# Kernel tuning notes

Hardware: AMD Instinct MI355X
Metric: run time of the kernel (lower is better)

The kernel has to match this reference:

```python
import jax, jax.numpy as jnp
import numpy as np

N = 8192
F_IN = 512
F_HID = 256
ALPHA = 0.2  # LeakyReLU negative slope
NEG_INF = -9e15


def gat_layer(h, adj, W, a):
    """Standard dense GraphAttentionLayer (pyGAT style).
    h: [N, F_in], adj: [N, N] (0/1), W: [F_in, F_out], a: [2*F_out, 1].
    """
    Wh = h @ W  # [N, F_out]
    f_out = W.shape[1]
    # e_ij = leakyrelu(a1 . Wh_i + a2 . Wh_j) via broadcasting
    e1 = Wh @ a[:f_out]      # [N, 1]
    e2 = Wh @ a[f_out:]      # [N, 1]
    e = jax.nn.leaky_relu(e1 + e2.T, negative_slope=ALPHA)  # [N, N]
    e = jnp.where(adj > 0, e, NEG_INF)
    att = jax.nn.softmax(e, axis=-1)  # masked row softmax
    return jax.nn.elu(att @ Wh)       # [N, F_out]


def setup_inputs() -> dict:
    key = jax.random.key(0)
    k_x, k_adj, k_w1, k_a1, k_w2, k_a2 = jax.random.split(key, 6)
    x = jax.random.normal(k_x, (N, F_IN), dtype=jnp.float32)
    # sparse random adjacency (~avg degree 16) + self loops
    adj = (jax.random.uniform(k_adj, (N, N)) < (16.0 / N)).astype(jnp.float32)
    adj = jnp.clip(adj + jnp.eye(N, dtype=jnp.float32), 0.0, 1.0)
    # Xavier-ish init for layer params
    W1 = jax.random.normal(k_w1, (F_IN, F_HID), dtype=jnp.float32) * (1.0 / np.sqrt(F_IN))
    a1 = jax.random.normal(k_a1, (2 * F_HID, 1), dtype=jnp.float32) * (1.0 / np.sqrt(2 * F_HID))
    W2 = jax.random.normal(k_w2, (F_HID, F_IN), dtype=jnp.float32) * (1.0 / np.sqrt(F_HID))
    a2 = jax.random.normal(k_a2, (2 * F_IN, 1), dtype=jnp.float32) * (1.0 / np.sqrt(2 * F_IN))
    return {"x": x, "adj": adj, "W1": W1, "a1": a1, "W2": W2, "a2": a2}


def reference(x, adj, W1, a1, W2, a2):
    enc = gat_layer(x, adj, W1, a1)    # encode: [N, F_HID]
    dec = gat_layer(enc, adj, W2, a2)  # decode: [N, F_IN]
    return (dec, enc)
```

## Files before the change

kernel.cpp:

```cpp
#include <hip/hip_runtime.h>
#include <hip/hip_bf16.h>

#define N_NODES 8192
#define F_IN    512
#define F_HID   256
#define ALPHA   0.2f
#define MAXDEG  64

using f32x4 = __attribute__((ext_vector_type(4))) float;
using f16x8 = __attribute__((ext_vector_type(8))) _Float16;
using f16x4 = __attribute__((ext_vector_type(4))) _Float16;

__global__ void conv_WT(const float* __restrict__ W1, const float* __restrict__ W2,
                        _Float16* __restrict__ W1T, _Float16* __restrict__ W2T,
                        const float* __restrict__ a2,
                        float* __restrict__ w2s, float* __restrict__ w2t,
                        float* __restrict__ stz) {
    const int tid = threadIdx.x;
    int gid = blockIdx.x * 256 + tid;
    if (gid < 2 * N_NODES) stz[gid] = 0.0f;

    if (blockIdx.x >= 256) {
        const int r = (blockIdx.x - 256) * 64 + (tid >> 2);
        const int q = tid & 3;
        float ss = 0.f, tt = 0.f;
        for (int n = q * 4; n < F_IN; n += 16) {
            f32x4 w  = *(const f32x4*)&W2[(size_t)r * F_IN + n];
            f32x4 as = *(const f32x4*)&a2[n];
            f32x4 at = *(const f32x4*)&a2[F_IN + n];
            #pragma unroll
            for (int j = 0; j < 4; ++j) { ss += w[j] * as[j]; tt += w[j] * at[j]; }
        }
        ss += __shfl_xor(ss, 1); ss += __shfl_xor(ss, 2);
        tt += __shfl_xor(tt, 1); tt += __shfl_xor(tt, 2);
        if (q == 0) { w2s[r] = ss; w2t[r] = tt; }
        return;
    }

    int t = blockIdx.x;
    const float* W; _Float16* WT; int K, N, kt, nt;
    if (t < 128) { W = W1; WT = W1T; K = 512; N = 256; kt = t & 15; nt = t >> 4; }
    else { t -= 128; W = W2; WT = W2T; K = 256; N = 512; kt = t & 7; nt = t >> 3; }
    __shared__ float Ws[32][33];
    const int tx = tid & 31, ty = tid >> 5;
    #pragma unroll
    for (int i = 0; i < 4; ++i)
        Ws[ty + 8 * i][tx] = W[(size_t)(kt * 32 + ty + 8 * i) * N + nt * 32 + tx];
    __syncthreads();
    #pragma unroll
    for (int i = 0; i < 4; ++i)
        WT[(size_t)(nt * 32 + ty + 8 * i) * K + kt * 32 + tx] = (_Float16)Ws[tx][ty + 8 * i];
}

__device__ inline void csr_row(const float* __restrict__ adj, int* __restrict__ cols,
                               int* __restrict__ cnt, int row, int lane) {
    const f32x4* arow = (const f32x4*)(adj + (size_t)row * N_NODES);
    int* crow = cols + (size_t)row * MAXDEG;
    int count = 0;
    const unsigned long long mlt = (1ULL << lane) - 1ULL;
    for (int base = 0; base < N_NODES; base += 512) {
        f32x4 v0 = __builtin_nontemporal_load(&arow[(base >> 2) + lane]);
        f32x4 v1 = __builtin_nontemporal_load(&arow[(base >> 2) + 64 + lane]);
        unsigned long long b0 = __ballot(v0[0] > 0.0f);
        unsigned long long b1 = __ballot(v0[1] > 0.0f);
        unsigned long long b2 = __ballot(v0[2] > 0.0f);
        unsigned long long b3 = __ballot(v0[3] > 0.0f);
        unsigned long long b4 = __ballot(v1[0] > 0.0f);
        unsigned long long b5 = __ballot(v1[1] > 0.0f);
        unsigned long long b6 = __ballot(v1[2] > 0.0f);
        unsigned long long b7 = __ballot(v1[3] > 0.0f);
        int o = count + __popcll(b0 & mlt) + __popcll(b1 & mlt)
                      + __popcll(b2 & mlt) + __popcll(b3 & mlt);
        int c0 = base + (lane << 2);
        if (v0[0] > 0.0f) { if (o < MAXDEG) crow[o] = c0;     o++; }
        if (v0[1] > 0.0f) { if (o < MAXDEG) crow[o] = c0 + 1; o++; }
        if (v0[2] > 0.0f) { if (o < MAXDEG) crow[o] = c0 + 2; o++; }
        if (v0[3] > 0.0f) { if (o < MAXDEG) crow[o] = c0 + 3; o++; }
        count += __popcll(b0) + __popcll(b1) + __popcll(b2) + __popcll(b3);
        o = count + __popcll(b4 & mlt) + __popcll(b5 & mlt)
                  + __popcll(b6 & mlt) + __popcll(b7 & mlt);
        int c1 = base + 256 + (lane << 2);
        if (v1[0] > 0.0f) { if (o < MAXDEG) crow[o] = c1;     o++; }
        if (v1[1] > 0.0f) { if (o < MAXDEG) crow[o] = c1 + 1; o++; }
        if (v1[2] > 0.0f) { if (o < MAXDEG) crow[o] = c1 + 2; o++; }
        if (v1[3] > 0.0f) { if (o < MAXDEG) crow[o] = c1 + 3; o++; }
        count += __popcll(b4) + __popcll(b5) + __popcll(b6) + __popcll(b7);
    }
    if (lane == 0) cnt[row] = count > MAXDEG ? MAXDEG : count;
}

__device__ inline void gemm1_tile(const float* __restrict__ x,
                                  const _Float16* __restrict__ W1T,
                                  _Float16* __restrict__ Wh1,
                                  const float* __restrict__ a1,
                                  float* __restrict__ s1, float* __restrict__ t1,
                                  int brow, int bcol) {
    const int LDT = 72;
    __shared__ _Float16 As[64 * LDT];
    __shared__ _Float16 Bs[64 * LDT];
    const int tid = threadIdx.x;
    const int wid = tid >> 6, lane = tid & 63;
    const int wr = (wid >> 1) * 32, wc = (wid & 1) * 32;
    const int sr = tid >> 3, skg = (tid & 7) * 8;

    f32x4 acc[2][2];
    #pragma unroll
    for (int m = 0; m < 2; ++m)
        #pragma unroll
        for (int n = 0; n < 2; ++n) acc[m][n] = f32x4{0.f, 0.f, 0.f, 0.f};

    for (int k0 = 0; k0 < F_IN; k0 += 64) {
        #pragma unroll
        for (int i = 0; i < 2; ++i) {
            int r = sr + i * 32;
            const f32x4* src = (const f32x4*)(x + (size_t)(brow + r) * F_IN + k0 + skg);
            f32x4 a0 = __builtin_nontemporal_load(src);
            f32x4 a1v = __builtin_nontemporal_load(src + 1);
            f16x8 av;
            #pragma unroll
            for (int j = 0; j < 4; ++j) { av[j] = (_Float16)a0[j]; av[4 + j] = (_Float16)a1v[j]; }
            *(f16x8*)&As[r * LDT + skg] = av;
            *(f16x8*)&Bs[r * LDT + skg] = *(const f16x8*)&W1T[(size_t)(bcol + r) * F_IN + k0 + skg];
        }
        __syncthreads();
        #pragma unroll
        for (int ks = 0; ks < 2; ++ks) {
            const int kb = ks * 32 + (lane >> 4) * 8;
            f16x8 af[2], bfr[2];
            #pragma unroll
            for (int m = 0; m < 2; ++m)
                af[m] = *(const f16x8*)&As[(wr + m * 16 + (lane & 15)) * LDT + kb];
            #pragma unroll
            for (int n = 0; n < 2; ++n)
                bfr[n] = *(const f16x8*)&Bs[(wc + n * 16 + (lane & 15)) * LDT + kb];
            #pragma unroll
            for (int m = 0; m < 2; ++m)
                #pragma unroll
                for (int n = 0; n < 2; ++n)
                    acc[m][n] = __builtin_amdgcn_mfma_f32_16x16x32_f16(
                        af[m], bfr[n], acc[m][n], 0, 0, 0);
        }
        __syncthreads();
    }
    const int c0 = bcol + wc + (lane & 15);
    float as0 = a1[c0],         as1 = a1[c0 + 16];
    float at0 = a1[F_HID + c0], at1 = a1[F_HID + c0 + 16];
    #pragma unroll
    for (int m = 0; m < 2; ++m) {
        #pragma unroll
        for (int j = 0; j < 4; ++j) {
            float vs = acc[m][0][j] * as0 + acc[m][1][j] * as1;
            float vt = acc[m][0][j] * at0 + acc[m][1][j] * at1;
            #pragma unroll
            for (int off = 1; off < 16; off <<= 1) {
                vs += __shfl_xor(vs, off);
                vt += __shfl_xor(vt, off);
            }
            if ((lane & 15) == 0) {
                int row = brow + wr + m * 16 + ((lane >> 4) << 2) + j;
                atomicAdd(s1 + row, vs);
                atomicAdd(t1 + row, vt);
            }
        }
        #pragma unroll
        for (int n = 0; n < 2; ++n) {
            int row = brow + wr + m * 16 + ((lane >> 4) << 2);
            int col = bcol + wc + n * 16 + (lane & 15);
            #pragma unroll
            for (int j = 0; j < 4; ++j)
                Wh1[(size_t)(row + j) * F_HID + col] = (_Float16)acc[m][n][j];
        }
    }
}

__global__ __launch_bounds__(256)
void csr_and_gemm1(const float* __restrict__ adj, int* __restrict__ cols,
                   int* __restrict__ cnt, const float* __restrict__ x,
                   const _Float16* __restrict__ W1T, _Float16* __restrict__ Wh1,
                   const float* __restrict__ a1,
                   float* __restrict__ s1, float* __restrict__ t1) {
    const int bid = blockIdx.x;
    const int g = bid / 5, r = bid % 5;
    if (r == 0) {
        gemm1_tile(x, W1T, Wh1, a1, s1, t1, (g >> 2) * 64, (g & 3) * 64);
    } else {
        const int cb = g * 4 + (r - 1);
        const int row = cb * 4 + (threadIdx.x >> 6);
        csr_row(adj, cols, cnt, row, threadIdx.x & 63);
    }
}

__global__ void aggregate_l1(const _Float16* __restrict__ Wh,
                             const int* __restrict__ cols, const int* __restrict__ cnt,
                             const float* __restrict__ s, const float* __restrict__ t,
                             const float* __restrict__ w2s, const float* __restrict__ w2t,
                             float* __restrict__ enc, _Float16* __restrict__ enc16,
                             float* __restrict__ s2, float* __restrict__ t2) {
    const int wid = threadIdx.x >> 6, lane = threadIdx.x & 63;
    const int row = blockIdx.x * 4 + wid;
    const int deg = cnt[row];
    __shared__ float pS[4][64];
    __shared__ int jS[4][64];
    int j = 0;
    float ev = -1e30f;
    if (lane < deg) {
        j = cols[(size_t)row * MAXDEG + lane];
        float z = s[row] + t[j];
        ev = z > 0.0f ? z : ALPHA * z;
    }
    float m = ev;
    #pragma unroll
    for (int off = 32; off > 0; off >>= 1) m = fmaxf(m, __shfl_xor(m, off));
    float ex = (lane < deg) ? __expf(ev - m) : 0.0f;
    float sum = ex;
    #pragma unroll
    for (int off = 32; off > 0; off >>= 1) sum += __shfl_xor(sum, off);
    pS[wid][lane] = ex / sum;
    jS[wid][lane] = j;
    __syncthreads();

    float acc[4] = {};
    const size_t lo = (size_t)lane * 4;
    int d = 0;
    for (; d + 4 <= deg; d += 4) {
        float p0 = pS[wid][d],     p1 = pS[wid][d + 1];
        float p2 = pS[wid][d + 2], p3 = pS[wid][d + 3];
        f16x4 v0 = *(const f16x4*)(Wh + (size_t)jS[wid][d] * F_HID + lo);
        f16x4 v1 = *(const f16x4*)(Wh + (size_t)jS[wid][d + 1] * F_HID + lo);
        f16x4 v2 = *(const f16x4*)(Wh + (size_t)jS[wid][d + 2] * F_HID + lo);
        f16x4 v3 = *(const f16x4*)(Wh + (size_t)jS[wid][d + 3] * F_HID + lo);
        #pragma unroll
        for (int jj = 0; jj < 4; ++jj)
            acc[jj] += p0 * (float)v0[jj] + p1 * (float)v1[jj]
                     + p2 * (float)v2[jj] + p3 * (float)v3[jj];
    }
    for (; d < deg; ++d) {
        float p = pS[wid][d];
        f16x4 w = *(const f16x4*)(Wh + (size_t)jS[wid][d] * F_HID + lo);
        #pragma unroll
        for (int jj = 0; jj < 4; ++jj) acc[jj] += p * (float)w[jj];
    }
    f32x4 o; f16x4 h;
    #pragma unroll
    for (int jj = 0; jj < 4; ++jj) {
        float v = acc[jj];
        float e = v > 0.0f ? v : (__expf(v) - 1.0f);
        o[jj] = e; h[jj] = (_Float16)e;
    }
    __builtin_nontemporal_store(o, (f32x4*)(enc + (size_t)row * F_HID + lo));
    *(f16x4*)(enc16 + (size_t)row * F_HID + lo) = h;

    f32x4 ws = *(const f32x4*)(w2s + lo);
    f32x4 wt = *(const f32x4*)(w2t + lo);
    float ps = 0.f, pt = 0.f;
    #pragma unroll
    for (int jj = 0; jj < 4; ++jj) { ps += o[jj] * ws[jj]; pt += o[jj] * wt[jj]; }
    #pragma unroll
    for (int off = 32; off > 0; off >>= 1) {
        ps += __shfl_xor(ps, off);
        pt += __shfl_xor(pt, off);
    }
    if (lane == 0) { s2[row] = ps; t2[row] = pt; }
}

__global__ void aggregate_l2pre(const _Float16* __restrict__ enc16,
                                const int* __restrict__ cols, const int* __restrict__ cnt,
                                const float* __restrict__ s, const float* __restrict__ t,
                                _Float16* __restrict__ aggE16) {
    const int wid = threadIdx.x >> 6, lane = threadIdx.x & 63;
    const int row = blockIdx.x * 4 + wid;
    const int deg = cnt[row];
    __shared__ float pS[4][64];
    __shared__ int jS[4][64];
    int j = 0;
    float ev = -1e30f;
    if (lane < deg) {
        j = cols[(size_t)row * MAXDEG + lane];
        float z = s[row] + t[j];
        ev = z > 0.0f ? z : ALPHA * z;
    }
    float m = ev;
    #pragma unroll
    for (int off = 32; off > 0; off >>= 1) m = fmaxf(m, __shfl_xor(m, off));
    float ex = (lane < deg) ? __expf(ev - m) : 0.0f;
    float sum = ex;
    #pragma unroll
    for (int off = 32; off > 0; off >>= 1) sum += __shfl_xor(sum, off);
    pS[wid][lane] = ex / sum;
    jS[wid][lane] = j;
    __syncthreads();

    float acc[4] = {};
    const size_t lo = (size_t)lane * 4;
    int d = 0;
    for (; d + 4 <= deg; d += 4) {
        float p0 = pS[wid][d],     p1 = pS[wid][d + 1];
        float p2 = pS[wid][d + 2], p3 = pS[wid][d + 3];
        f16x4 v0 = *(const f16x4*)(enc16 + (size_t)jS[wid][d] * F_HID + lo);
        f16x4 v1 = *(const f16x4*)(enc16 + (size_t)jS[wid][d + 1] * F_HID + lo);
        f16x4 v2 = *(const f16x4*)(enc16 + (size_t)jS[wid][d + 2] * F_HID + lo);
        f16x4 v3 = *(const f16x4*)(enc16 + (size_t)jS[wid][d + 3] * F_HID + lo);
        #pragma unroll
        for (int jj = 0; jj < 4; ++jj)
            acc[jj] += p0 * (float)v0[jj] + p1 * (float)v1[jj]
                     + p2 * (float)v2[jj] + p3 * (float)v3[jj];
    }
    for (; d < deg; ++d) {
        float p = pS[wid][d];
        f16x4 w = *(const f16x4*)(enc16 + (size_t)jS[wid][d] * F_HID + lo);
        #pragma unroll
        for (int jj = 0; jj < 4; ++jj) acc[jj] += p * (float)w[jj];
    }
    f16x4 h;
    #pragma unroll
    for (int jj = 0; jj < 4; ++jj) h[jj] = (_Float16)acc[jj];
    *(f16x4*)(aggE16 + (size_t)row * F_HID + lo) = h;
}

__global__ __launch_bounds__(256)
void gemm2e(const _Float16* __restrict__ A, const _Float16* __restrict__ BT,
            float* __restrict__ C) {
    const int LDT = 72, LDB = 264;
    __shared__ _Float16 As[128 * LDT];
    __shared__ _Float16 Bs[64 * LDB];
    const int tid = threadIdx.x;
    const int wid = tid >> 6, lane = tid & 63;
    const int brow = (blockIdx.x >> 3) * 128;
    const int bcol = (blockIdx.x & 7) * 64;
    const int wr = (wid >> 1) * 64, wc = (wid & 1) * 32;

    #pragma unroll
    for (int i = 0; i < 8; ++i) {
        int id = tid + i * 256;
        int r = id >> 5, kc = (id & 31) * 8;
        *(f16x8*)&Bs[r * LDB + kc] = *(const f16x8*)&BT[(size_t)(bcol + r) * F_HID + kc];
    }

    f32x4 acc[4][2];
    #pragma unroll
    for (int m = 0; m < 4; ++m)
        #pragma unroll
        for (int n = 0; n < 2; ++n) acc[m][n] = f32x4{0.f, 0.f, 0.f, 0.f};

    for (int k0 = 0; k0 < F_HID; k0 += 64) {
        #pragma unroll
        for (int i = 0; i < 4; ++i) {
            int id = tid + i * 256;
            int r = id >> 3, kc = (id & 7) * 8;
            *(f16x8*)&As[r * LDT + kc] = *(const f16x8*)&A[(size_t)(brow + r) * F_HID + k0 + kc];
        }
        __syncthreads();
        #pragma unroll
        for (int ks = 0; ks < 2; ++ks) {
            const int kb = ks * 32 + (lane >> 4) * 8;
            f16x8 af[4], bfr[2];
            #pragma unroll
            for (int m = 0; m < 4; ++m)
                af[m] = *(const f16x8*)&As[(wr + m * 16 + (lane & 15)) * LDT + kb];
            #pragma unroll
            for (int n = 0; n < 2; ++n)
                bfr[n] = *(const f16x8*)&Bs[(wc + n * 16 + (lane & 15)) * LDB + k0 + kb];
            #pragma unroll
            for (int m = 0; m < 4; ++m)
                #pragma unroll
                for (int n = 0; n < 2; ++n)
                    acc[m][n] = __builtin_amdgcn_mfma_f32_16x16x32_f16(
                        af[m], bfr[n], acc[m][n], 0, 0, 0);
        }
        __syncthreads();
    }
    #pragma unroll
    for (int m = 0; m < 4; ++m)
        #pragma unroll
        for (int n = 0; n < 2; ++n) {
            int row = brow + wr + m * 16 + ((lane >> 4) << 2);
            int col = bcol + wc + n * 16 + (lane & 15);
            #pragma unroll
            for (int j = 0; j < 4; ++j) {
                float v = acc[m][n][j];
                float e = v > 0.0f ? v : (__expf(v) - 1.0f);
                __builtin_nontemporal_store(e, &C[(size_t)(row + j) * F_IN + col]);
            }
        }
}

extern "C" void kernel_launch(void* const* d_in, const int* in_sizes, int n_in,
                              void* d_out, int out_size, void* d_ws, size_t ws_size,
                              hipStream_t stream) {
    (void)in_sizes; (void)n_in; (void)out_size; (void)ws_size;
    const float* x   = (const float*)d_in[0];
    const float* adj = (const float*)d_in[1];
    const float* W1  = (const float*)d_in[2];
    const float* a1  = (const float*)d_in[3];
    const float* W2  = (const float*)d_in[4];
    const float* a2  = (const float*)d_in[5];

    float* dec = (float*)d_out;
    float* enc = dec + (size_t)N_NODES * F_IN;

    int*      cols   = (int*)d_ws;
    int*      cnt    = cols + (size_t)N_NODES * MAXDEG;
    float*    s1     = (float*)(cnt + N_NODES);
    float*    t1     = s1 + N_NODES;
    float*    s2     = t1 + N_NODES;
    float*    t2     = s2 + N_NODES;
    float*    w2s    = t2 + N_NODES;
    float*    w2t    = w2s + F_HID;
    _Float16* Wh1    = (_Float16*)(w2t + F_HID);
    _Float16* enc16  = Wh1 + (size_t)N_NODES * F_HID;
    _Float16* aggE16 = enc16 + (size_t)N_NODES * F_HID;
    _Float16* W1T    = aggE16 + (size_t)N_NODES * F_HID;
    _Float16* W2T    = W1T + (size_t)F_HID * F_IN;

    conv_WT<<<260, 256, 0, stream>>>(W1, W2, W1T, W2T, a2, w2s, w2t, s1);

    csr_and_gemm1<<<2560, 256, 0, stream>>>(adj, cols, cnt, x, W1T, Wh1, a1, s1, t1);

    aggregate_l1<<<N_NODES / 4, 256, 0, stream>>>(Wh1, cols, cnt, s1, t1,
                                                  w2s, w2t, enc, enc16, s2, t2);

    aggregate_l2pre<<<N_NODES / 4, 256, 0, stream>>>(enc16, cols, cnt, s2, t2, aggE16);

    gemm2e<<<512, 256, 0, stream>>>(aggE16, W2T, dec);
}
```

Before: 108.0 us.

## Fuse layer-2 aggregation with output GEMM and split CSR build across kernels

Layer-2 neighbor aggregation and the W2 GEMM with ELU now run in one kernel. Each block aggregates 16 rows into LDS and multiplies them against W2T, so the aggE16 intermediate is no longer written to and read back from global memory, and one launch goes away. CSR construction is split: half the rows are scanned alongside GEMM1, and the other half are scanned inside the layer-1 aggregation kernel, which uses the indices straight from LDS. GEMM1 tiles are widened to 64x128. The trade-off is that the fused kernel runs only 512 blocks and every block reloads the full W2T from L2, and the serial per-wave gathers may limit parallelism.

```diff
diff --git a/kernel.cpp b/kernel.cpp
--- a/kernel.cpp
+++ b/kernel.cpp
@@ -11,11 +11,11 @@
 using f16x8 = __attribute__((ext_vector_type(8))) _Float16;
 using f16x4 = __attribute__((ext_vector_type(4))) _Float16;
 
-__global__ void conv_WT(const float* __restrict__ W1, const float* __restrict__ W2,
-                        _Float16* __restrict__ W1T, _Float16* __restrict__ W2T,
-                        const float* __restrict__ a2,
-                        float* __restrict__ w2s, float* __restrict__ w2t,
-                        float* __restrict__ stz) {
+__global__ void prep_kernel(const float* __restrict__ W1, const float* __restrict__ W2,
+                            _Float16* __restrict__ W1T, _Float16* __restrict__ W2T,
+                            const float* __restrict__ a2,
+                            float* __restrict__ w2s, float* __restrict__ w2t,
+                            float* __restrict__ stz) {
     const int tid = threadIdx.x;
     int gid = blockIdx.x * 256 + tid;
     if (gid < 2 * N_NODES) stz[gid] = 0.0f;
@@ -52,10 +52,9 @@
         WT[(size_t)(nt * 32 + ty + 8 * i) * K + kt * 32 + tx] = (_Float16)Ws[tx][ty + 8 * i];
 }
 
-__device__ inline void csr_row(const float* __restrict__ adj, int* __restrict__ cols,
-                               int* __restrict__ cnt, int row, int lane) {
+__device__ inline int csr_scan(const float* __restrict__ adj, int* __restrict__ crow,
+                               int* jLds, int row, int lane) {
     const f32x4* arow = (const f32x4*)(adj + (size_t)row * N_NODES);
-    int* crow = cols + (size_t)row * MAXDEG;
     int count = 0;
     const unsigned long long mlt = (1ULL << lane) - 1ULL;
     for (int base = 0; base < N_NODES; base += 512) {
@@ -72,21 +71,21 @@
         int o = count + __popcll(b0 & mlt) + __popcll(b1 & mlt)
                       + __popcll(b2 & mlt) + __popcll(b3 & mlt);
         int c0 = base + (lane << 2);
-        if (v0[0] > 0.0f) { if (o < MAXDEG) crow[o] = c0;     o++; }
-        if (v0[1] > 0.0f) { if (o < MAXDEG) crow[o] = c0 + 1; o++; }
-        if (v0[2] > 0.0f) { if (o < MAXDEG) crow[o] = c0 + 2; o++; }
-        if (v0[3] > 0.0f) { if (o < MAXDEG) crow[o] = c0 + 3; o++; }
+        if (v0[0] > 0.0f) { if (o < MAXDEG) { crow[o] = c0;     if (jLds) jLds[o] = c0;     } o++; }
+        if (v0[1] > 0.0f) { if (o < MAXDEG) { crow[o] = c0 + 1; if (jLds) jLds[o] = c0 + 1; } o++; }
+        if (v0[2] > 0.0f) { if (o < MAXDEG) { crow[o] = c0 + 2; if (jLds) jLds[o] = c0 + 2; } o++; }
+        if (v0[3] > 0.0f) { if (o < MAXDEG) { crow[o] = c0 + 3; if (jLds) jLds[o] = c0 + 3; } o++; }
         count += __popcll(b0) + __popcll(b1) + __popcll(b2) + __popcll(b3);
         o = count + __popcll(b4 & mlt) + __popcll(b5 & mlt)
                   + __popcll(b6 & mlt) + __popcll(b7 & mlt);
         int c1 = base + 256 + (lane << 2);
-        if (v1[0] > 0.0f) { if (o < MAXDEG) crow[o] = c1;     o++; }
-        if (v1[1] > 0.0f) { if (o < MAXDEG) crow[o] = c1 + 1; o++; }
-        if (v1[2] > 0.0f) { if (o < MAXDEG) crow[o] = c1 + 2; o++; }
-        if (v1[3] > 0.0f) { if (o < MAXDEG) crow[o] = c1 + 3; o++; }
+        if (v1[0] > 0.0f) { if (o < MAXDEG) { crow[o] = c1;     if (jLds) jLds[o] = c1;     } o++; }
+        if (v1[1] > 0.0f) { if (o < MAXDEG) { crow[o] = c1 + 1; if (jLds) jLds[o] = c1 + 1; } o++; }
+        if (v1[2] > 0.0f) { if (o < MAXDEG) { crow[o] = c1 + 2; if (jLds) jLds[o] = c1 + 2; } o++; }
+        if (v1[3] > 0.0f) { if (o < MAXDEG) { crow[o] = c1 + 3; if (jLds) jLds[o] = c1 + 3; } o++; }
         count += __popcll(b4) + __popcll(b5) + __popcll(b6) + __popcll(b7);
     }
-    if (lane == 0) cnt[row] = count > MAXDEG ? MAXDEG : count;
+    return count > MAXDEG ? MAXDEG : count;
 }
 
 __device__ inline void gemm1_tile(const float* __restrict__ x,
@@ -97,75 +96,85 @@
                                   int brow, int bcol) {
     const int LDT = 72;
     __shared__ _Float16 As[64 * LDT];
-    __shared__ _Float16 Bs[64 * LDT];
+    __shared__ _Float16 Bs[128 * LDT];
     const int tid = threadIdx.x;
     const int wid = tid >> 6, lane = tid & 63;
-    const int wr = (wid >> 1) * 32, wc = (wid & 1) * 32;
+    const int wr = (wid >> 1) * 32, wc = (wid & 1) * 64;
     const int sr = tid >> 3, skg = (tid & 7) * 8;
 
-    f32x4 acc[2][2];
+    f32x4 acc[2][4];
     #pragma unroll
     for (int m = 0; m < 2; ++m)
         #pragma unroll
-        for (int n = 0; n < 2; ++n) acc[m][n] = f32x4{0.f, 0.f, 0.f, 0.f};
+        for (int n = 0; n < 4; ++n) acc[m][n] = f32x4{0.f, 0.f, 0.f, 0.f};
 
     for (int k0 = 0; k0 < F_IN; k0 += 64) {
         #pragma unroll
         for (int i = 0; i < 2; ++i) {
             int r = sr + i * 32;
             const f32x4* src = (const f32x4*)(x + (size_t)(brow + r) * F_IN + k0 + skg);
-            f32x4 a0 = __builtin_nontemporal_load(src);
-            f32x4 a1v = __builtin_nontemporal_load(src + 1);
+            f32x4 a0 = src[0];
+            f32x4 a1v = src[1];
             f16x8 av;
             #pragma unroll
             for (int j = 0; j < 4; ++j) { av[j] = (_Float16)a0[j]; av[4 + j] = (_Float16)a1v[j]; }
             *(f16x8*)&As[r * LDT + skg] = av;
-            *(f16x8*)&Bs[r * LDT + skg] = *(const f16x8*)&W1T[(size_t)(bcol + r) * F_IN + k0 + skg];
+        }
+        #pragma unroll
+        for (int i = 0; i < 4; ++i) {
+            int r = sr + i * 32;
+            *(f16x8*)&Bs[r * LDT + skg] =
+                *(const f16x8*)&W1T[(size_t)(bcol + r) * F_IN + k0 + skg];
         }
         __syncthreads();
         #pragma unroll
         for (int ks = 0; ks < 2; ++ks) {
             const int kb = ks * 32 + (lane >> 4) * 8;
-            f16x8 af[2], bfr[2];
+            f16x8 af[2], bfr[4];
             #pragma unroll
             for (int m = 0; m < 2; ++m)
                 af[m] = *(const f16x8*)&As[(wr + m * 16 + (lane & 15)) * LDT + kb];
             #pragma unroll
-            for (int n = 0; n < 2; ++n)
+            for (int n = 0; n < 4; ++n)
                 bfr[n] = *(const f16x8*)&Bs[(wc + n * 16 + (lane & 15)) * LDT + kb];
             #pragma unroll
             for (int m = 0; m < 2; ++m)
                 #pragma unroll
-                for (int n = 0; n < 2; ++n)
+                for (int n = 0; n < 4; ++n)
                     acc[m][n] = __builtin_amdgcn_mfma_f32_16x16x32_f16(
                         af[m], bfr[n], acc[m][n], 0, 0, 0);
         }
         __syncthreads();
     }
-    const int c0 = bcol + wc + (lane & 15);
-    float as0 = a1[c0],         as1 = a1[c0 + 16];
-    float at0 = a1[F_HID + c0], at1 = a1[F_HID + c0 + 16];
+    const int cl = lane & 15;
+    float as[4], at[4];
+    #pragma unroll
+    for (int n = 0; n < 4; ++n) {
+        as[n] = a1[bcol + wc + n * 16 + cl];
+        at[n] = a1[F_HID + bcol + wc + n * 16 + cl];
+    }
     #pragma unroll
     for (int m = 0; m < 2; ++m) {
         #pragma unroll
         for (int j = 0; j < 4; ++j) {
-            float vs = acc[m][0][j] * as0 + acc[m][1][j] * as1;
-            float vt = acc[m][0][j] * at0 + acc[m][1][j] * at1;
+            float vs = 0.f, vt = 0.f;
+            #pragma unroll
+            for (int n = 0; n < 4; ++n) { vs += acc[m][n][j] * as[n]; vt += acc[m][n][j] * at[n]; }
             #pragma unroll
             for (int off = 1; off < 16; off <<= 1) {
                 vs += __shfl_xor(vs, off);
                 vt += __shfl_xor(vt, off);
             }
-            if ((lane & 15) == 0) {
+            if (cl == 0) {
                 int row = brow + wr + m * 16 + ((lane >> 4) << 2) + j;
                 atomicAdd(s1 + row, vs);
                 atomicAdd(t1 + row, vt);
             }
         }
         #pragma unroll
-        for (int n = 0; n < 2; ++n) {
+        for (int n = 0; n < 4; ++n) {
             int row = brow + wr + m * 16 + ((lane >> 4) << 2);
-            int col = bcol + wc + n * 16 + (lane & 15);
+            int col = bcol + wc + n * 16 + cl;
             #pragma unroll
             for (int j = 0; j < 4; ++j)
                 Wh1[(size_t)(row + j) * F_HID + col] = (_Float16)acc[m][n][j];
@@ -174,38 +183,52 @@
 }
 
 __global__ __launch_bounds__(256)
-void csr_and_gemm1(const float* __restrict__ adj, int* __restrict__ cols,
-                   int* __restrict__ cnt, const float* __restrict__ x,
-                   const _Float16* __restrict__ W1T, _Float16* __restrict__ Wh1,
-                   const float* __restrict__ a1,
-                   float* __restrict__ s1, float* __restrict__ t1) {
+void gemm1_csr(const float* __restrict__ adj, int* __restrict__ cols,
+               int* __restrict__ cnt, const float* __restrict__ x,
+               const _Float16* __restrict__ W1T, _Float16* __restrict__ Wh1,
+               const float* __restrict__ a1,
+               float* __restrict__ s1, float* __restrict__ t1) {
     const int bid = blockIdx.x;
     const int g = bid / 5, r = bid % 5;
     if (r == 0) {
-        gemm1_tile(x, W1T, Wh1, a1, s1, t1, (g >> 2) * 64, (g & 3) * 64);
+        gemm1_tile(x, W1T, Wh1, a1, s1, t1, (g & 127) * 64, (g >> 7) * 128);
     } else {
-        const int cb = g * 4 + (r - 1);
-        const int row = cb * 4 + (threadIdx.x >> 6);
-        csr_row(adj, cols, cnt, row, threadIdx.x & 63);
-    }
-}
-
-__global__ void aggregate_l1(const _Float16* __restrict__ Wh,
-                             const int* __restrict__ cols, const int* __restrict__ cnt,
-                             const float* __restrict__ s, const float* __restrict__ t,
-                             const float* __restrict__ w2s, const float* __restrict__ w2t,
-                             float* __restrict__ enc, _Float16* __restrict__ enc16,
-                             float* __restrict__ s2, float* __restrict__ t2) {
+        const int q = g * 4 + (r - 1);
+        const int row = q * 4 + (threadIdx.x >> 6);
+        const int lane = threadIdx.x & 63;
+        int deg = csr_scan(adj, cols + (size_t)row * MAXDEG, nullptr, row, lane);
+        if (lane == 0) cnt[row] = deg;
+    }
+}
+
+__global__ __launch_bounds__(256)
+void csr_agg1(const float* __restrict__ adj, int* __restrict__ cols,
+              int* __restrict__ cnt, const _Float16* __restrict__ Wh1,
+              const float* __restrict__ s1, const float* __restrict__ t1,
+              const float* __restrict__ w2s, const float* __restrict__ w2t,
+              float* __restrict__ enc, _Float16* __restrict__ enc16,
+              float* __restrict__ s2, float* __restrict__ t2) {
+    const int bid = blockIdx.x;
     const int wid = threadIdx.x >> 6, lane = threadIdx.x & 63;
-    const int row = blockIdx.x * 4 + wid;
-    const int deg = cnt[row];
+    const bool doCsr = !(bid & 1);
+    const int quad = doCsr ? 1024 + (bid >> 1) : (bid >> 1);
+    const int row = quad * 4 + wid;
+    __shared__ int jS[4][64];
     __shared__ float pS[4][64];
-    __shared__ int jS[4][64];
-    int j = 0;
+
+    int deg;
+    if (doCsr) {
+        deg = csr_scan(adj, cols + (size_t)row * MAXDEG, jS[wid], row, lane);
+        if (lane == 0) cnt[row] = deg;
+    } else {
+        deg = cnt[row];
+        if (lane < deg) jS[wid][lane] = cols[(size_t)row * MAXDEG + lane];
+    }
+
+    const float sI = s1[row];
     float ev = -1e30f;
     if (lane < deg) {
-        j = cols[(size_t)row * MAXDEG + lane];
-        float z = s[row] + t[j];
+        float z = sI + t1[jS[wid][lane]];
         ev = z > 0.0f ? z : ALPHA * z;
     }
     float m = ev;
@@ -216,8 +239,6 @@
     #pragma unroll
     for (int off = 32; off > 0; off >>= 1) sum += __shfl_xor(sum, off);
     pS[wid][lane] = ex / sum;
-    jS[wid][lane] = j;
-    __syncthreads();
 
     float acc[4] = {};
     const size_t lo = (size_t)lane * 4;
@@ -225,10 +246,10 @@
     for (; d + 4 <= deg; d += 4) {
         float p0 = pS[wid][d],     p1 = pS[wid][d + 1];
         float p2 = pS[wid][d + 2], p3 = pS[wid][d + 3];
-        f16x4 v0 = *(const f16x4*)(Wh + (size_t)jS[wid][d] * F_HID + lo);
-        f16x4 v1 = *(const f16x4*)(Wh + (size_t)jS[wid][d + 1] * F_HID + lo);
-        f16x4 v2 = *(const f16x4*)(Wh + (size_t)jS[wid][d + 2] * F_HID + lo);
-        f16x4 v3 = *(const f16x4*)(Wh + (size_t)jS[wid][d + 3] * F_HID + lo);
+        f16x4 v0 = *(const f16x4*)(Wh1 + (size_t)jS[wid][d] * F_HID + lo);
+        f16x4 v1 = *(const f16x4*)(Wh1 + (size_t)jS[wid][d + 1] * F_HID + lo);
+        f16x4 v2 = *(const f16x4*)(Wh1 + (size_t)jS[wid][d + 2] * F_HID + lo);
+        f16x4 v3 = *(const f16x4*)(Wh1 + (size_t)jS[wid][d + 3] * F_HID + lo);
         #pragma unroll
         for (int jj = 0; jj < 4; ++jj)
             acc[jj] += p0 * (float)v0[jj] + p1 * (float)v1[jj]
@@ -236,7 +257,7 @@
     }
     for (; d < deg; ++d) {
         float p = pS[wid][d];
-        f16x4 w = *(const f16x4*)(Wh + (size_t)jS[wid][d] * F_HID + lo);
+        f16x4 w = *(const f16x4*)(Wh1 + (size_t)jS[wid][d] * F_HID + lo);
         #pragma unroll
         for (int jj = 0; jj < 4; ++jj) acc[jj] += p * (float)w[jj];
     }
@@ -263,125 +284,99 @@
     if (lane == 0) { s2[row] = ps; t2[row] = pt; }
 }
 
-__global__ void aggregate_l2pre(const _Float16* __restrict__ enc16,
-                                const int* __restrict__ cols, const int* __restrict__ cnt,
-                                const float* __restrict__ s, const float* __restrict__ t,
-                                _Float16* __restrict__ aggE16) {
+__global__ __launch_bounds__(256)
+void l2_fused(const _Float16* __restrict__ enc16, const _Float16* __restrict__ W2T,
+              const int* __restrict__ cols, const int* __restrict__ cnt,
+              const float* __restrict__ s2, const float* __restrict__ t2,
+              float* __restrict__ dec) {
+    const int LDA = 264, LDB = 264;
+    __shared__ _Float16 aggE[16 * LDA];
+    __shared__ _Float16 Bs[64 * LDB];
+    const int base = blockIdx.x * 16;
     const int wid = threadIdx.x >> 6, lane = threadIdx.x & 63;
-    const int row = blockIdx.x * 4 + wid;
-    const int deg = cnt[row];
-    __shared__ float pS[4][64];
-    __shared__ int jS[4][64];
-    int j = 0;
-    float ev = -1e30f;
-    if (lane < deg) {
-        j = cols[(size_t)row * MAXDEG + lane];
-        float z = s[row] + t[j];
-        ev = z > 0.0f ? z : ALPHA * z;
-    }
-    float m = ev;
-    #pragma unroll
-    for (int off = 32; off > 0; off >>= 1) m = fmaxf(m, __shfl_xor(m, off));
-    float ex = (lane < deg) ? __expf(ev - m) : 0.0f;
-    float sum = ex;
-    #pragma unroll
-    for (int off = 32; off > 0; off >>= 1) sum += __shfl_xor(sum, off);
-    pS[wid][lane] = ex / sum;
-    jS[wid][lane] = j;
+
+    for (int rr = 0; rr < 4; ++rr) {
+        const int row = base + wid * 4 + rr;
+        const int deg = cnt[row];
+        const float sI = s2[row];
+        int j = 0;
+        float ev = -1e30f;
+        if (lane < deg) {
+            j = cols[(size_t)row * MAXDEG + lane];
+            float z = sI + t2[j];
+            ev = z > 0.0f ? z : ALPHA * z;
+        }
+        float m = ev;
+        #pragma unroll
+        for (int off = 32; off > 0; off >>= 1) m = fmaxf(m, __shfl_xor(m, off));
+        float ex = (lane < deg) ? __expf(ev - m) : 0.0f;
+        float sum = ex;
+        #pragma unroll
+        for (int off = 32; off > 0; off >>= 1) sum += __shfl_xor(sum, off);
+        float p = ex / sum;
+
+        float acc[4] = {};
+        const size_t lo = (size_t)lane * 4;
+        int d = 0;
+        for (; d + 4 <= deg; d += 4) {
+            float p0 = __shfl(p, d),     p1 = __shfl(p, d + 1);
+            float p2 = __shfl(p, d + 2), p3 = __shfl(p, d + 3);
+            int j0 = __shfl(j, d),     j1 = __shfl(j, d + 1);
+            int j2 = __shfl(j, d + 2), j3 = __shfl(j, d + 3);
+            f16x4 v0 = *(const f16x4*)(enc16 + (size_t)j0 * F_HID + lo);
+            f16x4 v1 = *(const f16x4*)(enc16 + (size_t)j1 * F_HID + lo);
+            f16x4 v2 = *(const f16x4*)(enc16 + (size_t)j2 * F_HID + lo);
+            f16x4 v3 = *(const f16x4*)(enc16 + (size_t)j3 * F_HID + lo);
+            #pragma unroll
+            for (int jj = 0; jj < 4; ++jj)
+                acc[jj] += p0 * (float)v0[jj] + p1 * (float)v1[jj]
+                         + p2 * (float)v2[jj] + p3 * (float)v3[jj];
+        }
+        for (; d < deg; ++d) {
+            float pd = __shfl(p, d);
+            int jd = __shfl(j, d);
+            f16x4 v = *(const f16x4*)(enc16 + (size_t)jd * F_HID + lo);
+            #pragma unroll
+            for (int jj = 0; jj < 4; ++jj) acc[jj] += pd * (float)v[jj];
+        }
+        f16x4 h;
+        #pragma unroll
+        for (int jj = 0; jj < 4; ++jj) h[jj] = (_Float16)acc[jj];
+        *(f16x4*)&aggE[(wid * 4 + rr) * LDA + lane * 4] = h;
+    }
     __syncthreads();
 
-    float acc[4] = {};
-    const size_t lo = (size_t)lane * 4;
-    int d = 0;
-    for (; d + 4 <= deg; d += 4) {
-        float p0 = pS[wid][d],     p1 = pS[wid][d + 1];
-        float p2 = pS[wid][d + 2], p3 = pS[wid][d + 3];
-        f16x4 v0 = *(const f16x4*)(enc16 + (size_t)jS[wid][d] * F_HID + lo);
-        f16x4 v1 = *(const f16x4*)(enc16 + (size_t)jS[wid][d + 1] * F_HID + lo);
-        f16x4 v2 = *(const f16x4*)(enc16 + (size_t)jS[wid][d + 2] * F_HID + lo);
-        f16x4 v3 = *(const f16x4*)(enc16 + (size_t)jS[wid][d + 3] * F_HID + lo);
-        #pragma unroll
-        for (int jj = 0; jj < 4; ++jj)
-            acc[jj] += p0 * (float)v0[jj] + p1 * (float)v1[jj]
-                     + p2 * (float)v2[jj] + p3 * (float)v3[jj];
-    }
-    for (; d < deg; ++d) {
-        float p = pS[wid][d];
-        f16x4 w = *(const f16x4*)(enc16 + (size_t)jS[wid][d] * F_HID + lo);
-        #pragma unroll
-        for (int jj = 0; jj < 4; ++jj) acc[jj] += p * (float)w[jj];
-    }
-    f16x4 h;
-    #pragma unroll
-    for (int jj = 0; jj < 4; ++jj) h[jj] = (_Float16)acc[jj];
-    *(f16x4*)(aggE16 + (size_t)row * F_HID + lo) = h;
-}
-
-__global__ __launch_bounds__(256)
-void gemm2e(const _Float16* __restrict__ A, const _Float16* __restrict__ BT,
-            float* __restrict__ C) {
-    const int LDT = 72, LDB = 264;
-    __shared__ _Float16 As[128 * LDT];
-    __shared__ _Float16 Bs[64 * LDB];
-    const int tid = threadIdx.x;
-    const int wid = tid >> 6, lane = tid & 63;
-    const int brow = (blockIdx.x >> 3) * 128;
-    const int bcol = (blockIdx.x & 7) * 64;
-    const int wr = (wid >> 1) * 64, wc = (wid & 1) * 32;
-
-    #pragma unroll
-    for (int i = 0; i < 8; ++i) {
-        int id = tid + i * 256;
-        int r = id >> 5, kc = (id & 31) * 8;
-        *(f16x8*)&Bs[r * LDB + kc] = *(const f16x8*)&BT[(size_t)(bcol + r) * F_HID + kc];
-    }
-
-    f32x4 acc[4][2];
-    #pragma unroll
-    for (int m = 0; m < 4; ++m)
-        #pragma unroll
-        for (int n = 0; n < 2; ++n) acc[m][n] = f32x4{0.f, 0.f, 0.f, 0.f};
-
-    for (int k0 = 0; k0 < F_HID; k0 += 64) {
-        #pragma unroll
-        for (int i = 0; i < 4; ++i) {
-            int id = tid + i * 256;
-            int r = id >> 3, kc = (id & 7) * 8;
-            *(f16x8*)&As[r * LDT + kc] = *(const f16x8*)&A[(size_t)(brow + r) * F_HID + k0 + kc];
+    f16x8 af[8];
+    #pragma unroll
+    for (int kf = 0; kf < 8; ++kf)
+        af[kf] = *(const f16x8*)&aggE[(lane & 15) * LDA + kf * 32 + (lane >> 4) * 8];
+
+    for (int ct = 0; ct < 8; ++ct) {
+        #pragma unroll
+        for (int i = 0; i < 8; ++i) {
+            int idx = threadIdx.x + i * 256;
+            int c = idx >> 5, kg = (idx & 31) * 8;
+            *(f16x8*)&Bs[c * LDB + kg] =
+                *(const f16x8*)&W2T[(size_t)(ct * 64 + c) * F_HID + kg];
         }
         __syncthreads();
-        #pragma unroll
-        for (int ks = 0; ks < 2; ++ks) {
-            const int kb = ks * 32 + (lane >> 4) * 8;
-            f16x8 af[4], bfr[2];
-            #pragma unroll
-            for (int m = 0; m < 4; ++m)
-                af[m] = *(const f16x8*)&As[(wr + m * 16 + (lane & 15)) * LDT + kb];
-            #pragma unroll
-            for (int n = 0; n < 2; ++n)
-                bfr[n] = *(const f16x8*)&Bs[(wc + n * 16 + (lane & 15)) * LDB + k0 + kb];
-            #pragma unroll
-            for (int m = 0; m < 4; ++m)
-                #pragma unroll
-                for (int n = 0; n < 2; ++n)
-                    acc[m][n] = __builtin_amdgcn_mfma_f32_16x16x32_f16(
-                        af[m], bfr[n], acc[m][n], 0, 0, 0);
+        f32x4 oacc = f32x4{0.f, 0.f, 0.f, 0.f};
+        #pragma unroll
+        for (int kf = 0; kf < 8; ++kf) {
+            f16x8 bf = *(const f16x8*)&Bs[(wid * 16 + (lane & 15)) * LDB
+                                          + kf * 32 + (lane >> 4) * 8];
+            oacc = __builtin_amdgcn_mfma_f32_16x16x32_f16(af[kf], bf, oacc, 0, 0, 0);
+        }
+        const int col = ct * 64 + wid * 16 + (lane & 15);
+        const int row0 = base + ((lane >> 4) << 2);
+        #pragma unroll
+        for (int jj = 0; jj < 4; ++jj) {
+            float v = oacc[jj];
+            float e = v > 0.0f ? v : (__expf(v) - 1.0f);
+            __builtin_nontemporal_store(e, &dec[(size_t)(row0 + jj) * F_IN + col]);
         }
         __syncthreads();
     }
-    #pragma unroll
-    for (int m = 0; m < 4; ++m)
-        #pragma unroll
-        for (int n = 0; n < 2; ++n) {
-            int row = brow + wr + m * 16 + ((lane >> 4) << 2);
-            int col = bcol + wc + n * 16 + (lane & 15);
-            #pragma unroll
-            for (int j = 0; j < 4; ++j) {
-                float v = acc[m][n][j];
-                float e = v > 0.0f ? v : (__expf(v) - 1.0f);
-                __builtin_nontemporal_store(e, &C[(size_t)(row + j) * F_IN + col]);
-            }
-        }
 }
 
 extern "C" void kernel_launch(void* const* d_in, const int* in_sizes, int n_in,
@@ -398,28 +393,25 @@
     float* dec = (float*)d_out;
     float* enc = dec + (size_t)N_NODES * F_IN;
 
-    int*      cols   = (int*)d_ws;
-    int*      cnt    = cols + (size_t)N_NODES * MAXDEG;
-    float*    s1     = (float*)(cnt + N_NODES);
-    float*    t1     = s1 + N_NODES;
-    float*    s2     = t1 + N_NODES;
-    float*    t2     = s2 + N_NODES;
-    float*    w2s    = t2 + N_NODES;
-    float*    w2t    = w2s + F_HID;
-    _Float16* Wh1    = (_Float16*)(w2t + F_HID);
-    _Float16* enc16  = Wh1 + (size_t)N_NODES * F_HID;
-    _Float16* aggE16 = enc16 + (size_t)N_NODES * F_HID;
-    _Float16* W1T    = aggE16 + (size_t)N_NODES * F_HID;
-    _Float16* W2T    = W1T + (size_t)F_HID * F_IN;
-
-    conv_WT<<<260, 256, 0, stream>>>(W1, W2, W1T, W2T, a2, w2s, w2t, s1);
-
-    csr_and_gemm1<<<2560, 256, 0, stream>>>(adj, cols, cnt, x, W1T, Wh1, a1, s1, t1);
-
-    aggregate_l1<<<N_NODES / 4, 256, 0, stream>>>(Wh1, cols, cnt, s1, t1,
-                                                  w2s, w2t, enc, enc16, s2, t2);
-
-    aggregate_l2pre<<<N_NODES / 4, 256, 0, stream>>>(enc16, cols, cnt, s2, t2, aggE16);
-
-    gemm2e<<<512, 256, 0, stream>>>(aggE16, W2T, dec);
-}
+    int*      cols  = (int*)d_ws;
+    int*      cnt   = cols + (size_t)N_NODES * MAXDEG;
+    float*    s1    = (float*)(cnt + N_NODES);
+    float*    t1    = s1 + N_NODES;
+    float*    s2    = t1 + N_NODES;
+    float*    t2    = s2 + N_NODES;
+    float*    w2s   = t2 + N_NODES;
+    float*    w2t   = w2s + F_HID;
+    _Float16* Wh1   = (_Float16*)(w2t + F_HID);
+    _Float16* enc16 = Wh1 + (size_t)N_NODES * F_HID;
+    _Float16* W1T   = enc16 + (size_t)N_NODES * F_HID;
+    _Float16* W2T   = W1T + (size_t)F_HID * F_IN;
+
+    prep_kernel<<<260, 256, 0, stream>>>(W1, W2, W1T, W2T, a2, w2s, w2t, s1);
+
+    gemm1_csr<<<1280, 256, 0, stream>>>(adj, cols, cnt, x, W1T, Wh1, a1, s1, t1);
+
+    csr_agg1<<<2048, 256, 0, stream>>>(adj, cols, cnt, Wh1, s1, t1,
+                                       w2s, w2t, enc, enc16, s2, t2);
+
+    l2_fused<<<N_NODES / 16, 256, 0, stream>>>(enc16, W2T, cols, cnt, s2, t2, dec);
+}
```

After: 120.0 us. 11.1% more time.

## Widen gemm1 tiles to 64x128 and place GEMM blocks before CSR blocks

Applied to the files above, without the earlier changes.

The fused CSR+GEMM1 kernel now uses 64x128 output tiles (4 N-subtiles per warp), which halves the number of GEMM blocks and halves how often x is re-read and converted. GEMM blocks are now grouped at the start of the grid instead of interleaved one in every five with the CSR-building blocks. Nontemporal loads of x are replaced with plain loads, and conv_WT is renamed. The wider tile uses more registers and shared memory, and the new grid order changes how the GEMM and the memory-bound adjacency scan overlap.

```diff
diff --git a/kernel.cpp b/kernel.cpp
--- a/kernel.cpp
+++ b/kernel.cpp
@@ -11,11 +11,11 @@
 using f16x8 = __attribute__((ext_vector_type(8))) _Float16;
 using f16x4 = __attribute__((ext_vector_type(4))) _Float16;
 
-__global__ void conv_WT(const float* __restrict__ W1, const float* __restrict__ W2,
-                        _Float16* __restrict__ W1T, _Float16* __restrict__ W2T,
-                        const float* __restrict__ a2,
-                        float* __restrict__ w2s, float* __restrict__ w2t,
-                        float* __restrict__ stz) {
+__global__ void prep_kernel(const float* __restrict__ W1, const float* __restrict__ W2,
+                            _Float16* __restrict__ W1T, _Float16* __restrict__ W2T,
+                            const float* __restrict__ a2,
+                            float* __restrict__ w2s, float* __restrict__ w2t,
+                            float* __restrict__ stz) {
     const int tid = threadIdx.x;
     int gid = blockIdx.x * 256 + tid;
     if (gid < 2 * N_NODES) stz[gid] = 0.0f;
@@ -97,75 +97,85 @@
                                   int brow, int bcol) {
     const int LDT = 72;
     __shared__ _Float16 As[64 * LDT];
-    __shared__ _Float16 Bs[64 * LDT];
+    __shared__ _Float16 Bs[128 * LDT];
     const int tid = threadIdx.x;
     const int wid = tid >> 6, lane = tid & 63;
-    const int wr = (wid >> 1) * 32, wc = (wid & 1) * 32;
+    const int wr = (wid >> 1) * 32, wc = (wid & 1) * 64;
     const int sr = tid >> 3, skg = (tid & 7) * 8;
 
-    f32x4 acc[2][2];
+    f32x4 acc[2][4];
     #pragma unroll
     for (int m = 0; m < 2; ++m)
         #pragma unroll
-        for (int n = 0; n < 2; ++n) acc[m][n] = f32x4{0.f, 0.f, 0.f, 0.f};
+        for (int n = 0; n < 4; ++n) acc[m][n] = f32x4{0.f, 0.f, 0.f, 0.f};
 
     for (int k0 = 0; k0 < F_IN; k0 += 64) {
         #pragma unroll
         for (int i = 0; i < 2; ++i) {
             int r = sr + i * 32;
             const f32x4* src = (const f32x4*)(x + (size_t)(brow + r) * F_IN + k0 + skg);
-            f32x4 a0 = __builtin_nontemporal_load(src);
-            f32x4 a1v = __builtin_nontemporal_load(src + 1);
+            f32x4 a0 = src[0];
+            f32x4 a1v = src[1];
             f16x8 av;
             #pragma unroll
             for (int j = 0; j < 4; ++j) { av[j] = (_Float16)a0[j]; av[4 + j] = (_Float16)a1v[j]; }
             *(f16x8*)&As[r * LDT + skg] = av;
-            *(f16x8*)&Bs[r * LDT + skg] = *(const f16x8*)&W1T[(size_t)(bcol + r) * F_IN + k0 + skg];
+        }
+        #pragma unroll
+        for (int i = 0; i < 4; ++i) {
+            int r = sr + i * 32;
+            *(f16x8*)&Bs[r * LDT + skg] =
+                *(const f16x8*)&W1T[(size_t)(bcol + r) * F_IN + k0 + skg];
         }
         __syncthreads();
         #pragma unroll
         for (int ks = 0; ks < 2; ++ks) {
             const int kb = ks * 32 + (lane >> 4) * 8;
-            f16x8 af[2], bfr[2];
+            f16x8 af[2], bfr[4];
             #pragma unroll
             for (int m = 0; m < 2; ++m)
                 af[m] = *(const f16x8*)&As[(wr + m * 16 + (lane & 15)) * LDT + kb];
             #pragma unroll
-            for (int n = 0; n < 2; ++n)
+            for (int n = 0; n < 4; ++n)
                 bfr[n] = *(const f16x8*)&Bs[(wc + n * 16 + (lane & 15)) * LDT + kb];
             #pragma unroll
             for (int m = 0; m < 2; ++m)
                 #pragma unroll
-                for (int n = 0; n < 2; ++n)
+                for (int n = 0; n < 4; ++n)
                     acc[m][n] = __builtin_amdgcn_mfma_f32_16x16x32_f16(
                         af[m], bfr[n], acc[m][n], 0, 0, 0);
         }
         __syncthreads();
     }
-    const int c0 = bcol + wc + (lane & 15);
-    float as0 = a1[c0],         as1 = a1[c0 + 16];
-    float at0 = a1[F_HID + c0], at1 = a1[F_HID + c0 + 16];
+    const int cl = lane & 15;
+    float as[4], at[4];
+    #pragma unroll
+    for (int n = 0; n < 4; ++n) {
+        as[n] = a1[bcol + wc + n * 16 + cl];
+        at[n] = a1[F_HID + bcol + wc + n * 16 + cl];
+    }
     #pragma unroll
     for (int m = 0; m < 2; ++m) {
         #pragma unroll
         for (int j = 0; j < 4; ++j) {
-            float vs = acc[m][0][j] * as0 + acc[m][1][j] * as1;
-            float vt = acc[m][0][j] * at0 + acc[m][1][j] * at1;
+            float vs = 0.f, vt = 0.f;
+            #pragma unroll
+            for (int n = 0; n < 4; ++n) { vs += acc[m][n][j] * as[n]; vt += acc[m][n][j] * at[n]; }
             #pragma unroll
             for (int off = 1; off < 16; off <<= 1) {
                 vs += __shfl_xor(vs, off);
                 vt += __shfl_xor(vt, off);
             }
-            if ((lane & 15) == 0) {
+            if (cl == 0) {
                 int row = brow + wr + m * 16 + ((lane >> 4) << 2) + j;
                 atomicAdd(s1 + row, vs);
                 atomicAdd(t1 + row, vt);
             }
         }
         #pragma unroll
-        for (int n = 0; n < 2; ++n) {
+        for (int n = 0; n < 4; ++n) {
             int row = brow + wr + m * 16 + ((lane >> 4) << 2);
-            int col = bcol + wc + n * 16 + (lane & 15);
+            int col = bcol + wc + n * 16 + cl;
             #pragma unroll
             for (int j = 0; j < 4; ++j)
                 Wh1[(size_t)(row + j) * F_HID + col] = (_Float16)acc[m][n][j];
@@ -180,12 +190,11 @@
                    const float* __restrict__ a1,
                    float* __restrict__ s1, float* __restrict__ t1) {
     const int bid = blockIdx.x;
-    const int g = bid / 5, r = bid % 5;
-    if (r == 0) {
-        gemm1_tile(x, W1T, Wh1, a1, s1, t1, (g >> 2) * 64, (g & 3) * 64);
+    if (bid < 256) {
+        gemm1_tile(x, W1T, Wh1, a1, s1, t1, (bid & 127) * 64, (bid >> 7) * 128);
     } else {
-        const int cb = g * 4 + (r - 1);
-        const int row = cb * 4 + (threadIdx.x >> 6);
+        const int q = bid - 256;
+        const int row = q * 4 + (threadIdx.x >> 6);
         csr_row(adj, cols, cnt, row, threadIdx.x & 63);
     }
 }
@@ -412,9 +421,9 @@
     _Float16* W1T    = aggE16 + (size_t)N_NODES * F_HID;
     _Float16* W2T    = W1T + (size_t)F_HID * F_IN;
 
-    conv_WT<<<260, 256, 0, stream>>>(W1, W2, W1T, W2T, a2, w2s, w2t, s1);
-
-    csr_and_gemm1<<<2560, 256, 0, stream>>>(adj, cols, cnt, x, W1T, Wh1, a1, s1, t1);
+    prep_kernel<<<260, 256, 0, stream>>>(W1, W2, W1T, W2T, a2, w2s, w2t, s1);
+
+    csr_and_gemm1<<<2304, 256, 0, stream>>>(adj, cols, cnt, x, W1T, Wh1, a1, s1, t1);
 
     aggregate_l1<<<N_NODES / 4, 256, 0, stream>>>(Wh1, cols, cnt, s1, t1,
                                                   w2s, w2t, enc, enc16, s2, t2);
```

Measured after the change: 100.3 us. 1.08x faster.
